# Performance work log

Measured on AMD Instinct MI355X. Metric: run time of the kernel, lower is better.

Reference implementation:

```python
import jax, jax.numpy as jnp
import numpy as np

NUM_CLASSES = 19
EPS = 1e-8  # torch cosine_similarity eps


def setup_inputs() -> dict:
    key = jax.random.key(0)
    k1, k2 = jax.random.split(key)
    inputs = jax.random.normal(k1, (8, 256, 128, 128), dtype=jnp.float32)  # (B, D, H, W)
    targets = jax.random.randint(k2, (8, 128, 128), 0, NUM_CLASSES)        # (B, H, W)
    return {"inputs": inputs, "targets": targets}


def reference(inputs, targets):
    B, D, H, W = inputs.shape
    C = NUM_CLASSES
    # (N, D) pixel embeddings and (N,) labels
    feats = jnp.transpose(inputs, (0, 2, 3, 1)).reshape(-1, D)
    labels = targets.reshape(-1)

    # per-class centroids: sum of embeddings / max(count, 1)  (matches sum_pixel = max(mask.sum(), 1))
    counts = jax.ops.segment_sum(jnp.ones(labels.shape, jnp.float32), labels, num_segments=C)  # (C,)
    sums = jax.ops.segment_sum(feats, labels, num_segments=C)                                   # (C, D)
    centers = sums / jnp.maximum(counts, 1.0)[:, None]
    present = counts > 0  # classes absent from the batch are skipped in both loss terms

    # ---- sim_loss: sum over present classes of mean_{pixels of class i} (1 - cos(center_i, feat)) ----
    cen_px = centers[labels]                                   # (N, D)
    dot = jnp.sum(feats * cen_px, axis=1)
    n_f = jnp.sqrt(jnp.sum(feats * feats, axis=1))
    n_c = jnp.sqrt(jnp.sum(cen_px * cen_px, axis=1))
    cos_px = dot / jnp.maximum(n_f * n_c, EPS)
    per_class = jax.ops.segment_sum(1.0 - cos_px, labels, num_segments=C) / jnp.maximum(counts, 1.0)
    sim_loss = jnp.sum(jnp.where(present, per_class, 0.0))

    # ---- diff_loss: for each present i, mean_j over all C classes of
    #      (1 - cos(center_j, center_i)) if j == i else relu(cos(center_j, center_i)) ----
    n_cen = jnp.sqrt(jnp.sum(centers * centers, axis=1))       # (C,)
    S = (centers @ centers.T) / jnp.maximum(n_cen[:, None] * n_cen[None, :], EPS)  # (C, C)
    eye = jnp.eye(C, dtype=bool)
    per_pair = jnp.where(eye, 1.0 - S, jnp.maximum(S, 0.0))    # row i = losses vs class i
    per_i = jnp.mean(per_pair, axis=1)                          # mean reduction over C rows
    diff_loss = jnp.sum(jnp.where(present, per_i, 0.0))

    return jnp.reshape(diff_loss + sim_loss, (1,))  # torch returns a shape-(1,) tensor
```

## Files before the change

kernel.cpp:

```cpp
#include <hip/hip_runtime.h>
#include <math.h>

#define D_DIM 256
#define HW 16384
#define C 19
#define N_PX 131072
#define EPS 1e-8f

#define S_SC  1048576.0f
#define IS_S  (1.0f/1048576.0f)
#define U_SC  16777216.0f
#define IS_U  (1.0f/16777216.0f)

#define OFF_S    0
#define OFF_U    4864
#define OFF_CNT  9728
#define WS_ZERO  9760
#define OFF_PART 9760
#define PSTRIDE  9760
#define G1       512

__global__ void k0_zero(int* __restrict__ ws) {
    int i = blockIdx.x * blockDim.x + threadIdx.x;
    if (i < WS_ZERO) ws[i] = 0;
}

__global__ __launch_bounds__(256) void k1_pass(const float* __restrict__ in,
                                               const int* __restrict__ tgt,
                                               int* __restrict__ wsi) {
    __shared__ int sS[C * 257];
    __shared__ int sU[C * 257];
    __shared__ int s_cnt[C];
    __shared__ __align__(16) float s_nfp[128 * 4];
    const int tid = threadIdx.x;
    const int q   = tid & 63;
    const int dq  = tid >> 6;

    for (int i = tid; i < C * 257; i += 256) { sS[i] = 0; sU[i] = 0; }
    if (tid < C) s_cnt[tid] = 0;
    __syncthreads();

    const int px0 = blockIdx.x << 8;
    const int b   = px0 >> 14;

    #pragma unroll
    for (int r = 0; r < 2; ++r) {
        const int hwq = (px0 & (HW - 1)) + (r << 7) + (q << 1);
        const int p   = px0 + (r << 7) + (q << 1);
        const int la = tgt[p], lb = tgt[p + 1];
        if (dq == 0) { atomicAdd(&s_cnt[la], 1); atomicAdd(&s_cnt[lb], 1); }

        const float* base = in + (((size_t)(b * D_DIM + (dq << 6))) << 14) + hwq;

        float nfa = 0.f, nfb = 0.f;
        #pragma unroll
        for (int g = 0; g < 8; ++g) {
            float2 v[8];
            #pragma unroll
            for (int j = 0; j < 8; ++j)
                v[j] = *(const float2*)(base + ((size_t)(g * 8 + j) << 14));
            #pragma unroll
            for (int j = 0; j < 8; ++j) {
                nfa += v[j].x * v[j].x; nfb += v[j].y * v[j].y;
            }
        }
        s_nfp[(q << 3) + dq]     = nfa;
        s_nfp[(q << 3) + 4 + dq] = nfb;
        __syncthreads();

        const float4 na4 = *(const float4*)&s_nfp[q << 3];
        const float4 nb4 = *(const float4*)&s_nfp[(q << 3) + 4];
        const float nfs_a = na4.x + na4.y + na4.z + na4.w;
        const float nfs_b = nb4.x + nb4.y + nb4.z + nb4.w;
        const float sa = nfs_a > 0.f ? U_SC / sqrtf(nfs_a) : 0.f;
        const float sb = nfs_b > 0.f ? U_SC / sqrtf(nfs_b) : 0.f;

        #pragma unroll
        for (int g = 0; g < 8; ++g) {
            float2 v[8];
            #pragma unroll
            for (int j = 0; j < 8; ++j)
                v[j] = *(const float2*)(base + ((size_t)(g * 8 + j) << 14));
            #pragma unroll
            for (int j = 0; j < 8; ++j) {
                const int dd = (dq << 6) + g * 8 + j;
                atomicAdd(&sS[la * 257 + dd], __float2int_rn(v[j].x * S_SC));
                atomicAdd(&sS[lb * 257 + dd], __float2int_rn(v[j].y * S_SC));
                atomicAdd(&sU[la * 257 + dd], __float2int_rn(v[j].x * sa));
                atomicAdd(&sU[lb * 257 + dd], __float2int_rn(v[j].y * sb));
            }
        }
        __syncthreads();
    }

    int* __restrict__ row = wsi + OFF_PART + (size_t)blockIdx.x * PSTRIDE;
    for (int i = tid; i < C * 256; i += 256) {
        int c = i >> 8, d = i & 255;
        row[OFF_S + i] = sS[c * 257 + d];
        row[OFF_U + i] = sU[c * 257 + d];
    }
    if (tid < C)                 row[OFF_CNT + tid] = s_cnt[tid];
    else if (tid < 32)           row[OFF_CNT + tid] = 0;
}

__global__ __launch_bounds__(256) void k1b_reduce(int* __restrict__ wsi) {
    const int col4 = blockIdx.x * 256 + threadIdx.x;
    if (col4 >= PSTRIDE / 4) return;
    const int4* base = (const int4*)(wsi + OFF_PART)
                     + (size_t)blockIdx.y * 16 * (PSTRIDE / 4) + col4;
    int4 acc = {0, 0, 0, 0};
    #pragma unroll
    for (int r = 0; r < 16; ++r) {
        int4 v = base[(size_t)r * (PSTRIDE / 4)];
        acc.x += v.x; acc.y += v.y; acc.z += v.z; acc.w += v.w;
    }
    atomicAdd(&wsi[col4 * 4 + 0], acc.x);
    atomicAdd(&wsi[col4 * 4 + 1], acc.y);
    atomicAdd(&wsi[col4 * 4 + 2], acc.z);
    atomicAdd(&wsi[col4 * 4 + 3], acc.w);
}

__global__ __launch_bounds__(512) void k2_final(const int* __restrict__ wsi,
                                                float* __restrict__ out) {
    __shared__ __align__(16) float s_cen[C * 260];
    __shared__ __align__(16) float s_u[C * 260];
    __shared__ float s_nc[C];
    __shared__ float s_cntf[C];
    __shared__ float s_pair[C * C];
    __shared__ float s_sim[C];
    const int tid = threadIdx.x;

    if (tid < C) s_cntf[tid] = (float)wsi[OFF_CNT + tid];
    __syncthreads();
    for (int i = tid; i < C * 256; i += 512) {
        int c = i >> 8, d = i & 255;
        float icnt = 1.f / fmaxf(s_cntf[c], 1.f);
        s_cen[c * 260 + d] = (float)wsi[OFF_S + i] * IS_S * icnt;
        s_u[c * 260 + d]   = (float)wsi[OFF_U + i] * IS_U;
    }
    __syncthreads();
    if (tid < C) {
        float nsq = 0.f;
        for (int d = 0; d < D_DIM; ++d) {
            float x = s_cen[tid * 260 + d];
            nsq += x * x;
        }
        s_nc[tid] = sqrtf(nsq);
    }
    __syncthreads();
    if (tid < C * C) {
        int i = tid / C, j = tid % C;
        const float4* ci = (const float4*)&s_cen[i * 260];
        const float4* cj = (const float4*)&s_cen[j * 260];
        float dot = 0.f;
        #pragma unroll 8
        for (int k = 0; k < 64; ++k) {
            float4 a = ci[k], bb = cj[k];
            dot += a.x * bb.x + a.y * bb.y + a.z * bb.z + a.w * bb.w;
        }
        float S = dot / fmaxf(s_nc[i] * s_nc[j], EPS);
        s_pair[tid] = (i == j) ? (1.f - S) : fmaxf(S, 0.f);
    } else if (tid >= 384 && tid < 384 + C) {
        int i = tid - 384;
        const float4* ci = (const float4*)&s_cen[i * 260];
        const float4* ui = (const float4*)&s_u[i * 260];
        float dot = 0.f;
        #pragma unroll 8
        for (int k = 0; k < 64; ++k) {
            float4 a = ci[k], bb = ui[k];
            dot += a.x * bb.x + a.y * bb.y + a.z * bb.z + a.w * bb.w;
        }
        s_sim[i] = (s_cntf[i] > 0.f)
                 ? (1.f - dot / fmaxf(s_nc[i] * s_cntf[i], EPS)) : 0.f;
    }
    __syncthreads();
    if (tid < C) {
        float row = 0.f;
        for (int j = 0; j < C; ++j) row += s_pair[tid * C + j];
        s_pair[tid * C] = (s_cntf[tid] > 0.f) ? (row * (1.f / (float)C)) : 0.f;
    }
    __syncthreads();
    if (tid == 0) {
        float tot = 0.f;
        for (int i = 0; i < C; ++i) tot += s_pair[i * C] + s_sim[i];
        out[0] = tot;
    }
}

extern "C" void kernel_launch(void* const* d_in, const int* in_sizes, int n_in,
                              void* d_out, int out_size, void* d_ws, size_t ws_size,
                              hipStream_t stream) {
    const float* in  = (const float*)d_in[0];
    const int*   tgt = (const int*)d_in[1];
    float* out = (float*)d_out;
    int*   wsi = (int*)d_ws;

    k0_zero<<<39, 256, 0, stream>>>(wsi);
    k1_pass<<<G1, 256, 0, stream>>>(in, tgt, wsi);
    k1b_reduce<<<dim3(10, 32), 256, 0, stream>>>(wsi);
    k2_final<<<1, 512, 0, stream>>>(wsi, out);
}
```

Before: 229.9 us.

## Hold per-thread feature slices in registers to avoid second global read pass

Remaps threads so each handles 4 pixels across 32 interleaved channels, loading all values once as float4 into registers instead of reading the input twice. Per-pixel norms are now reduced with wave shuffles rather than through shared memory and barriers, and labels are read as int4. This halves global traffic and removes two barriers per iteration, at the cost of much higher register pressure (128 floats held live, with launch bounds requesting 2 blocks per SM) and a different LDS atomic access pattern.

```diff
diff --git a/kernel.cpp b/kernel.cpp
--- a/kernel.cpp
+++ b/kernel.cpp
@@ -25,16 +25,15 @@
     if (i < WS_ZERO) ws[i] = 0;
 }
 
-__global__ __launch_bounds__(256) void k1_pass(const float* __restrict__ in,
-                                               const int* __restrict__ tgt,
-                                               int* __restrict__ wsi) {
+__global__ __launch_bounds__(256, 2) void k1_pass(const float* __restrict__ in,
+                                                  const int* __restrict__ tgt,
+                                                  int* __restrict__ wsi) {
     __shared__ int sS[C * 257];
     __shared__ int sU[C * 257];
     __shared__ int s_cnt[C];
-    __shared__ __align__(16) float s_nfp[128 * 4];
     const int tid = threadIdx.x;
-    const int q   = tid & 63;
-    const int dq  = tid >> 6;
+    const int dq  = tid & 7;
+    const int qq  = tid >> 3;
 
     for (int i = tid; i < C * 257; i += 256) { sS[i] = 0; sU[i] = 0; }
     if (tid < C) s_cnt[tid] = 0;
@@ -42,56 +41,58 @@
 
     const int px0 = blockIdx.x << 8;
     const int b   = px0 >> 14;
+    const float* bbase = in + (((size_t)(b * D_DIM + dq)) << 14);
 
     #pragma unroll
     for (int r = 0; r < 2; ++r) {
-        const int hwq = (px0 & (HW - 1)) + (r << 7) + (q << 1);
-        const int p   = px0 + (r << 7) + (q << 1);
-        const int la = tgt[p], lb = tgt[p + 1];
-        if (dq == 0) { atomicAdd(&s_cnt[la], 1); atomicAdd(&s_cnt[lb], 1); }
-
-        const float* base = in + (((size_t)(b * D_DIM + (dq << 6))) << 14) + hwq;
-
-        float nfa = 0.f, nfb = 0.f;
-        #pragma unroll
-        for (int g = 0; g < 8; ++g) {
-            float2 v[8];
-            #pragma unroll
-            for (int j = 0; j < 8; ++j)
-                v[j] = *(const float2*)(base + ((size_t)(g * 8 + j) << 14));
-            #pragma unroll
-            for (int j = 0; j < 8; ++j) {
-                nfa += v[j].x * v[j].x; nfb += v[j].y * v[j].y;
-            }
-        }
-        s_nfp[(q << 3) + dq]     = nfa;
-        s_nfp[(q << 3) + 4 + dq] = nfb;
-        __syncthreads();
-
-        const float4 na4 = *(const float4*)&s_nfp[q << 3];
-        const float4 nb4 = *(const float4*)&s_nfp[(q << 3) + 4];
-        const float nfs_a = na4.x + na4.y + na4.z + na4.w;
-        const float nfs_b = nb4.x + nb4.y + nb4.z + nb4.w;
-        const float sa = nfs_a > 0.f ? U_SC / sqrtf(nfs_a) : 0.f;
-        const float sb = nfs_b > 0.f ? U_SC / sqrtf(nfs_b) : 0.f;
-
-        #pragma unroll
-        for (int g = 0; g < 8; ++g) {
-            float2 v[8];
-            #pragma unroll
-            for (int j = 0; j < 8; ++j)
-                v[j] = *(const float2*)(base + ((size_t)(g * 8 + j) << 14));
-            #pragma unroll
-            for (int j = 0; j < 8; ++j) {
-                const int dd = (dq << 6) + g * 8 + j;
-                atomicAdd(&sS[la * 257 + dd], __float2int_rn(v[j].x * S_SC));
-                atomicAdd(&sS[lb * 257 + dd], __float2int_rn(v[j].y * S_SC));
-                atomicAdd(&sU[la * 257 + dd], __float2int_rn(v[j].x * sa));
-                atomicAdd(&sU[lb * 257 + dd], __float2int_rn(v[j].y * sb));
-            }
-        }
-        __syncthreads();
-    }
+        const int hwq = (px0 & (HW - 1)) + (r << 7) + (qq << 2);
+        const int p   = px0 + (r << 7) + (qq << 2);
+        const int4 lab = *(const int4*)(tgt + p);
+        if (dq == 0) {
+            atomicAdd(&s_cnt[lab.x], 1); atomicAdd(&s_cnt[lab.y], 1);
+            atomicAdd(&s_cnt[lab.z], 1); atomicAdd(&s_cnt[lab.w], 1);
+        }
+
+        const float* base = bbase + hwq;
+        float4 v[32];
+        #pragma unroll
+        for (int g = 0; g < 32; ++g)
+            v[g] = *(const float4*)(base + ((size_t)g << 17));
+
+        float4 nf = {0.f, 0.f, 0.f, 0.f};
+        #pragma unroll
+        for (int g = 0; g < 32; ++g) {
+            nf.x += v[g].x * v[g].x; nf.y += v[g].y * v[g].y;
+            nf.z += v[g].z * v[g].z; nf.w += v[g].w * v[g].w;
+        }
+        #pragma unroll
+        for (int m = 1; m <= 4; m <<= 1) {
+            nf.x += __shfl_xor(nf.x, m, 64);
+            nf.y += __shfl_xor(nf.y, m, 64);
+            nf.z += __shfl_xor(nf.z, m, 64);
+            nf.w += __shfl_xor(nf.w, m, 64);
+        }
+        const float sa = nf.x > 0.f ? U_SC / sqrtf(nf.x) : 0.f;
+        const float sb = nf.y > 0.f ? U_SC / sqrtf(nf.y) : 0.f;
+        const float sc = nf.z > 0.f ? U_SC / sqrtf(nf.z) : 0.f;
+        const float sd = nf.w > 0.f ? U_SC / sqrtf(nf.w) : 0.f;
+
+        const int rowa = lab.x * 257, rowb = lab.y * 257,
+                  rowc = lab.z * 257, rowd = lab.w * 257;
+        #pragma unroll
+        for (int g = 0; g < 32; ++g) {
+            const int dd = (g << 3) + dq;
+            atomicAdd(&sS[rowa + dd], __float2int_rn(v[g].x * S_SC));
+            atomicAdd(&sS[rowb + dd], __float2int_rn(v[g].y * S_SC));
+            atomicAdd(&sS[rowc + dd], __float2int_rn(v[g].z * S_SC));
+            atomicAdd(&sS[rowd + dd], __float2int_rn(v[g].w * S_SC));
+            atomicAdd(&sU[rowa + dd], __float2int_rn(v[g].x * sa));
+            atomicAdd(&sU[rowb + dd], __float2int_rn(v[g].y * sb));
+            atomicAdd(&sU[rowc + dd], __float2int_rn(v[g].z * sc));
+            atomicAdd(&sU[rowd + dd], __float2int_rn(v[g].w * sd));
+        }
+    }
+    __syncthreads();
 
     int* __restrict__ row = wsi + OFF_PART + (size_t)blockIdx.x * PSTRIDE;
     for (int i = tid; i < C * 256; i += 256) {
```

Measured after the change: 217.6 us. 5.4% less time.
